# Kernel optimization log

Measured on AMD Instinct MI355X. Metric: run time of the kernel, lower is better.

Reference implementation:

```python
import jax, jax.numpy as jnp
import numpy as np

N_NODES = 50000
N_EDGES = 1600000
N_PAIRS = 4096
IN_N, IN_E = 32, 8
H, OE, ON = 4, 8, 32  # heads, out_edge_feats, out_node_feats
L = 4  # layers


def setup_inputs() -> dict:
    key = jax.random.key(0)
    ks = jax.random.split(key, 20)
    s = 0.1
    return {
        "x": jax.random.normal(ks[0], (N_NODES, IN_N), jnp.float32),
        "e": jax.random.normal(ks[1], (N_EDGES, IN_E), jnp.float32),
        "W_ni": jax.random.normal(ks[2], (L, IN_N, H * OE), jnp.float32) * s,
        "W_nj": jax.random.normal(ks[3], (L, IN_N, H * OE), jnp.float32) * s,
        "W_fij": jax.random.normal(ks[4], (L, IN_E, H * OE), jnp.float32) * s,
        "b_edge": jax.random.normal(ks[5], (L, H * OE), jnp.float32) * s,
        "attn": jax.random.normal(ks[6], (L, H, OE), jnp.float32) * s,
        "W_node": jax.random.normal(ks[7], (L, IN_N, H * ON), jnp.float32) * s,
        "W1": jax.random.normal(ks[8], (2 * L * ON, 128), jnp.float32) * s,
        "b1": jax.random.normal(ks[9], (128,), jnp.float32) * s,
        "W2": jax.random.normal(ks[10], (128, 1), jnp.float32) * s,
        "b2": jax.random.normal(ks[11], (1,), jnp.float32) * s,
        "src": jax.random.randint(ks[12], (N_EDGES,), 0, N_NODES, jnp.int32),
        "dst": jax.random.randint(ks[13], (N_EDGES,), 0, N_NODES, jnp.int32),
        "users": jax.random.randint(ks[14], (N_PAIRS,), 0, N_NODES, jnp.int32),
        "items": jax.random.randint(ks[15], (N_PAIRS,), 0, N_NODES, jnp.int32),
    }


def _egat_layer(h, e, src, dst, W_ni, W_nj, W_fij, b_edge, attn, W_node, n_nodes):
    # per-edge edge features: f_ni[src] + f_nj[dst] + f_fij + bias  -> (E, H*OE)
    f = (h @ W_ni)[src] + (h @ W_nj)[dst] + e @ W_fij + b_edge
    f_out = jax.nn.leaky_relu(f).reshape(-1, H, OE)          # (E, H, OE)
    logits = jnp.einsum("ehd,hd->eh", f_out, attn)           # (E, H)
    # edge softmax over incoming edges of each dst node
    mx = jax.ops.segment_max(logits, dst, num_segments=n_nodes)
    z = jnp.exp(logits - mx[dst])
    denom = jax.ops.segment_sum(z, dst, num_segments=n_nodes)
    a = z / denom[dst]                                        # (E, H)
    hh = (h @ W_node).reshape(n_nodes, H, ON)                 # (N, H, ON)
    msg = hh[src] * a[:, :, None]                             # (E, H, ON)
    return jax.ops.segment_sum(msg, dst, num_segments=n_nodes)  # (N, H, ON)


def reference(x, e, W_ni, W_nj, W_fij, b_edge, attn, W_node, W1, b1, W2, b2,
              src, dst, users, items):
    n_nodes = x.shape[0]
    states = []
    h = x
    for l in range(L):
        agg = _egat_layer(h, e, src, dst, W_ni[l], W_nj[l], W_fij[l],
                          b_edge[l], attn[l], W_node[l], n_nodes)
        h = jax.nn.elu(agg.sum(axis=1))  # sum heads, ELU -> (N, ON)
        states.append(h)
    states = jnp.concatenate(states, axis=1)                  # (N, L*ON)
    z = jnp.concatenate([states[users], states[items]], axis=1)  # (B, 2*L*ON)
    z = jax.nn.relu(z @ W1 + b1)
    out = jax.nn.sigmoid(z @ W2 + b2)
    return out[:, 0]
```

## Files before the change

kernel.cpp:

```cpp
#include <hip/hip_runtime.h>
#include <math.h>


static __device__ inline unsigned short f2bf(float f) {
  unsigned x = __float_as_uint(f);
  unsigned r = x + 0x7fffu + ((x >> 16) & 1u);
  return (unsigned short)(r >> 16);
}
static __device__ inline unsigned pack2bf(float lo, float hi) {
  return (unsigned)f2bf(lo) | ((unsigned)f2bf(hi) << 16);
}
static __device__ inline float bf_lo(unsigned u) {
  return __uint_as_float(u << 16);
}
static __device__ inline float bf_hi(unsigned u) {
  return __uint_as_float(u & 0xffff0000u);
}


__global__ void zero_ints(int* __restrict__ p, int n) {
  int i = blockIdx.x * blockDim.x + threadIdx.x;
  if (i < n) p[i] = 0;
}

__global__ void histogram(const int* __restrict__ dst, int* __restrict__ hist,
                          int n_edges) {
  int e = blockIdx.x * blockDim.x + threadIdx.x;
  if (e < n_edges) atomicAdd(&hist[dst[e]], 1);
}

__global__ void scan_block(const int* __restrict__ hist, int* __restrict__ partial,
                           int* __restrict__ blocksum, int n) {
  __shared__ int buf[1024];
  int tid = threadIdx.x;
  int g = blockIdx.x * 1024 + tid;
  int v = (g < n) ? hist[g] : 0;
  buf[tid] = v;
  __syncthreads();
  for (int off = 1; off < 1024; off <<= 1) {
    int t = (tid >= off) ? buf[tid - off] : 0;
    __syncthreads();
    buf[tid] += t;
    __syncthreads();
  }
  if (g < n) partial[g] = buf[tid] - v;
  if (tid == 1023) blocksum[blockIdx.x] = buf[1023];
}

__global__ void scan_sums(int* __restrict__ blocksum, int nb) {
  if (threadIdx.x == 0 && blockIdx.x == 0) {
    int run = 0;
    for (int i = 0; i < nb; i++) {
      int t = blocksum[i];
      blocksum[i] = run;
      run += t;
    }
    blocksum[nb] = run;
  }
}

__global__ void scan_add(int* __restrict__ partial ,
                         const int* __restrict__ blocksum,
                         int* __restrict__ cursor, int n, int nb) {
  int g = blockIdx.x * blockDim.x + threadIdx.x;
  if (g < n) {
    int val = partial[g] + blocksum[g >> 10];
    partial[g] = val;
    cursor[g] = val;
  }
  if (g == 0) partial[n] = blocksum[nb];
}

#define FILL_NR 8
__global__ void fill_rec(const int* __restrict__ dst, const int* __restrict__ src,
                         int* __restrict__ cursor, int2* __restrict__ rec,
                         int n_edges, int seg) {
  int range = blockIdx.x % FILL_NR;
  int group = blockIdx.x / FILL_NR;
  int ngroups = gridDim.x / FILL_NR;
  int lo = range * seg;
  int hi = lo + seg;
  int stride = ngroups * blockDim.x;
  for (int k = group * blockDim.x + threadIdx.x; k < n_edges; k += stride) {
    int d = dst[k];
    if (d >= lo && d < hi) {
      int p = atomicAdd(&cursor[d], 1);
      rec[p] = make_int2(src[k], k);
    }
  }
}

__global__ void dst_fill(const int* __restrict__ row_off, int* __restrict__ dst_s,
                         int n_nodes) {
  int n = blockIdx.x * blockDim.x + threadIdx.x;
  if (n >= n_nodes) return;
  int b = row_off[n], e = row_off[n + 1];
  for (int k = b; k < e; k++) dst_s[k] = n;
}

__global__ void expand_e(const int2* __restrict__ rec, const float* __restrict__ e,
                         uint4* __restrict__ e_s, int n_edges) {
  int k = blockIdx.x * blockDim.x + threadIdx.x;
  if (k >= n_edges) return;
  int eid = rec[k].y;
  const float4* ep = (const float4*)(e + (size_t)eid * 8);
  float4 a = ep[0], b = ep[1];
  uint4 r;
  r.x = pack2bf(a.x, a.y); r.y = pack2bf(a.z, a.w);
  r.z = pack2bf(b.x, b.y); r.w = pack2bf(b.z, b.w);
  e_s[k] = r;
}


__global__ void node_proj(const float* __restrict__ h,
                          const float* __restrict__ Wni,
                          const float* __restrict__ Wnj,
                          const float* __restrict__ Wnode,
                          const float* __restrict__ bE,
                          unsigned short* __restrict__ fni,
                          unsigned short* __restrict__ cdst,
                          unsigned short* __restrict__ hh, int n_nodes) {
  int wave = (blockIdx.x * blockDim.x + threadIdx.x) >> 6;
  int lane = threadIdx.x & 63;
  int nwaves = (gridDim.x * blockDim.x) >> 6;
  int j = lane & 31;
  const float* Wsel = (lane < 32) ? Wni : Wnj;
  for (int n = wave; n < n_nodes; n += nwaves) {
    const float* hrow = h + (size_t)n * 32;
    float a0 = 0.f, a1 = 0.f, a2 = 0.f;
#pragma unroll
    for (int k = 0; k < 32; k++) {
      float hv = hrow[k];
      a0 += hv * Wsel[k * 32 + j];
      a1 += hv * Wnode[k * 128 + lane];
      a2 += hv * Wnode[k * 128 + lane + 64];
    }
    if (lane < 32) fni[(size_t)n * 32 + j] = f2bf(a0);
    else           cdst[(size_t)n * 32 + j] = f2bf(a0 + bE[j]);
    hh[(size_t)n * 128 + lane] = f2bf(a1);
    hh[(size_t)n * 128 + lane + 64] = f2bf(a2);
  }
}

__global__ void edge_z(const int2* __restrict__ rec,
                       const int* __restrict__ dst_s,
                       const uint4* __restrict__ e_s,
                       const unsigned short* __restrict__ fni,
                       const unsigned short* __restrict__ cdst,
                       const float* __restrict__ Wf,
                       const float* __restrict__ attn,
                       float4* __restrict__ zrec, int n_edges) {
  __shared__ float wfl[256];
  __shared__ float atl[32];
  int tid = threadIdx.x;
  wfl[tid] = Wf[tid];
  if (tid < 32) atl[tid] = attn[tid];
  __syncthreads();
  int k = blockIdx.x * blockDim.x + tid;
  if (k >= n_edges) return;
  int s = rec[k].x, d = dst_s[k];
  uint4 ep = e_s[k];
  float ev[8];
  ev[0] = bf_lo(ep.x); ev[1] = bf_hi(ep.x);
  ev[2] = bf_lo(ep.y); ev[3] = bf_hi(ep.y);
  ev[4] = bf_lo(ep.z); ev[5] = bf_hi(ep.z);
  ev[6] = bf_lo(ep.w); ev[7] = bf_hi(ep.w);
  const uint4* fr = (const uint4*)(fni + (size_t)s * 32);
  const uint4* cr = (const uint4*)(cdst + (size_t)d * 32);
  float f[32];
#pragma unroll
  for (int q = 0; q < 4; q++) {
    uint4 ua = fr[q], ub = cr[q];
    const unsigned* uap = (const unsigned*)&ua;
    const unsigned* ubp = (const unsigned*)&ub;
#pragma unroll
    for (int c = 0; c < 4; c++) {
      int jj = q * 8 + c * 2;
      f[jj]     = bf_lo(uap[c]) + bf_lo(ubp[c]);
      f[jj + 1] = bf_hi(uap[c]) + bf_hi(ubp[c]);
    }
  }
#pragma unroll
  for (int kk = 0; kk < 8; kk++) {
    float ek = ev[kk];
#pragma unroll
    for (int j4 = 0; j4 < 8; j4++) {
      float4 w = ((const float4*)wfl)[kk * 8 + j4];
      f[j4 * 4 + 0] = fmaf(ek, w.x, f[j4 * 4 + 0]);
      f[j4 * 4 + 1] = fmaf(ek, w.y, f[j4 * 4 + 1]);
      f[j4 * 4 + 2] = fmaf(ek, w.z, f[j4 * 4 + 2]);
      f[j4 * 4 + 3] = fmaf(ek, w.w, f[j4 * 4 + 3]);
    }
  }
  float lg[4] = {0.f, 0.f, 0.f, 0.f};
#pragma unroll
  for (int jj = 0; jj < 32; jj++) {
    float t = f[jj];
    t = (t >= 0.f) ? t : 0.01f * t;
    lg[jj >> 3] = fmaf(t, atl[jj], lg[jj >> 3]);
  }
  zrec[k] = make_float4(__expf(lg[0]), __expf(lg[1]),
                        __expf(lg[2]), __expf(lg[3]));
}

__global__ void node_agg(const float4* __restrict__ zrec,
                         const int2* __restrict__ rec,
                         const int* __restrict__ row_off,
                         const unsigned* __restrict__ hh,
                         float* __restrict__ hcur,
                         float* __restrict__ states,
                         int l, int n_nodes) {
  __shared__ float zw[4][64 * 4];
  __shared__ int sw[4][64];
  int wid = threadIdx.x >> 6;
  int lane = threadIdx.x & 63;
  int n = (blockIdx.x * blockDim.x + threadIdx.x) >> 6;
  if (n >= n_nodes) return;
  int base = row_off[n], end = row_off[n + 1];
  int head = lane >> 4;
  float* zwf = zw[wid];
  int* swp = sw[wid];
  float accx = 0.f, accy = 0.f;
  float sz0 = 0.f, sz1 = 0.f, sz2 = 0.f, sz3 = 0.f;

  for (int chunk = base; chunk < end; chunk += 64) {
    int k = chunk + lane;
    float4 zv4 = make_float4(0.f, 0.f, 0.f, 0.f);
    int sv = 0;
    if (k < end) { zv4 = zrec[k]; sv = rec[k].x; }
    ((float4*)zwf)[lane] = zv4;
    swp[lane] = sv;
    sz0 += zv4.x; sz1 += zv4.y; sz2 += zv4.z; sz3 += zv4.w;
    int cnt = min(64, end - chunk);

    int ee = 0;
    for (; ee + 8 <= cnt; ee += 8) {
      unsigned u[8];
      float zl[8];
#pragma unroll
      for (int i = 0; i < 8; i++) {
        int ss = __builtin_amdgcn_readfirstlane(swp[ee + i]);
        zl[i] = zwf[(ee + i) * 4 + head];
        u[i] = hh[(size_t)ss * 64 + lane];
      }
#pragma unroll
      for (int i = 0; i < 8; i++) {
        accx = fmaf(bf_lo(u[i]), zl[i], accx);
        accy = fmaf(bf_hi(u[i]), zl[i], accy);
      }
    }
    for (; ee < cnt; ee++) {
      int ss = __builtin_amdgcn_readfirstlane(swp[ee]);
      float zv = zwf[ee * 4 + head];
      unsigned u = hh[(size_t)ss * 64 + lane];
      accx = fmaf(bf_lo(u), zv, accx);
      accy = fmaf(bf_hi(u), zv, accy);
    }
  }

#pragma unroll
  for (int off = 32; off > 0; off >>= 1) {
    sz0 += __shfl_xor(sz0, off); sz1 += __shfl_xor(sz1, off);
    sz2 += __shfl_xor(sz2, off); sz3 += __shfl_xor(sz3, off);
  }
  float dh = (head == 0) ? sz0 : (head == 1) ? sz1 : (head == 2) ? sz2 : sz3;

  float vx = 0.f, vy = 0.f;
  if (dh > 0.f) { vx = accx / dh; vy = accy / dh; }
  vx += __shfl_xor(vx, 16); vx += __shfl_xor(vx, 32);
  vy += __shfl_xor(vy, 16); vy += __shfl_xor(vy, 32);
  if (lane < 16) {
    float rx = (vx > 0.f) ? vx : expm1f(vx);
    float ry = (vy > 0.f) ? vy : expm1f(vy);
    float2 r = make_float2(rx, ry);
    ((float2*)(hcur + (size_t)n * 32))[lane] = r;
    ((float2*)(states + (size_t)n * 128 + l * 32))[lane] = r;
  }
}

__global__ void mlp_head(const float* __restrict__ states,
                         const int* __restrict__ users, const int* __restrict__ items,
                         const float* __restrict__ W1, const float* __restrict__ b1,
                         const float* __restrict__ W2, const float* __restrict__ b2,
                         float* __restrict__ out, int n_pairs) {
  __shared__ float zin[256];
  __shared__ float red[2];
  int p = blockIdx.x;
  if (p >= n_pairs) return;
  int t = threadIdx.x;
  int u = users[p], it = items[p];
  zin[t] = states[(size_t)u * 128 + t];
  zin[t + 128] = states[(size_t)it * 128 + t];
  __syncthreads();
  float acc = b1[t];
#pragma unroll 8
  for (int i = 0; i < 256; i++) acc += zin[i] * W1[i * 128 + t];
  acc = acc > 0.f ? acc : 0.f;
  float c = acc * W2[t];
#pragma unroll
  for (int off = 32; off > 0; off >>= 1) c += __shfl_down(c, off);
  if ((t & 63) == 0) red[t >> 6] = c;
  __syncthreads();
  if (t == 0) {
    float sum = red[0] + red[1] + b2[0];
    out[p] = 1.f / (1.f + expf(-sum));
  }
}


extern "C" void kernel_launch(void* const* d_in, const int* in_sizes, int n_in,
                              void* d_out, int out_size, void* d_ws, size_t ws_size,
                              hipStream_t stream) {
  const float* x     = (const float*)d_in[0];
  const float* e     = (const float*)d_in[1];
  const float* W_ni  = (const float*)d_in[2];
  const float* W_nj  = (const float*)d_in[3];
  const float* W_fij = (const float*)d_in[4];
  const float* b_e   = (const float*)d_in[5];
  const float* attn  = (const float*)d_in[6];
  const float* W_nd  = (const float*)d_in[7];
  const float* W1    = (const float*)d_in[8];
  const float* b1    = (const float*)d_in[9];
  const float* W2    = (const float*)d_in[10];
  const float* b2    = (const float*)d_in[11];
  const int* src   = (const int*)d_in[12];
  const int* dst   = (const int*)d_in[13];
  const int* users = (const int*)d_in[14];
  const int* items = (const int*)d_in[15];
  float* out = (float*)d_out;

  int n_nodes = in_sizes[0] / 32;
  int n_edges = in_sizes[12];
  int n_pairs = in_sizes[14];

  char* wsb = (char*)d_ws;
  size_t off = 0;
  auto alloc = [&](size_t bytes) {
    char* p = wsb + off;
    off = (off + bytes + 255) & ~(size_t)255;
    return p;
  };
  float*          hcur   = (float*)alloc((size_t)n_nodes * 32 * 4);
  float*          states = (float*)alloc((size_t)n_nodes * 128 * 4);
  unsigned short* fni    = (unsigned short*)alloc((size_t)n_nodes * 32 * 2);
  unsigned short* cdst   = (unsigned short*)alloc((size_t)n_nodes * 32 * 2);
  unsigned short* hh     = (unsigned short*)alloc((size_t)n_nodes * 128 * 2);
  uint4*          e_s    = (uint4*)alloc((size_t)n_edges * 16);
  float4*         zrec   = (float4*)alloc((size_t)n_edges * 16);
  int2*           rec    = (int2*)alloc((size_t)n_edges * 8);
  int*            dst_s  = (int*)alloc((size_t)n_edges * 4);
  int*            row_off  = (int*)alloc(((size_t)n_nodes + 8) * 4);
  int*            blocksum = (int*)alloc(256 * 4);
  int* hist   = (int*)zrec;
  int* cursor = (int*)((char*)zrec + (size_t)(n_nodes + 16) * 4);

  int nb = (n_nodes + 1023) / 1024;
  int seg = (n_nodes + FILL_NR - 1) / FILL_NR;
  zero_ints<<<(n_nodes + 255) / 256, 256, 0, stream>>>(hist, n_nodes);
  histogram<<<(n_edges + 255) / 256, 256, 0, stream>>>(dst, hist, n_edges);
  scan_block<<<nb, 1024, 0, stream>>>(hist, row_off, blocksum, n_nodes);
  scan_sums<<<1, 64, 0, stream>>>(blocksum, nb);
  scan_add<<<(n_nodes + 255) / 256, 256, 0, stream>>>(row_off, blocksum, cursor,
                                                      n_nodes, nb);
  fill_rec<<<2048, 256, 0, stream>>>(dst, src, cursor, rec, n_edges, seg);
  dst_fill<<<(n_nodes + 255) / 256, 256, 0, stream>>>(row_off, dst_s, n_nodes);
  expand_e<<<(n_edges + 255) / 256, 256, 0, stream>>>(rec, e, e_s, n_edges);

  for (int l = 0; l < 4; l++) {
    const float* hin = (l == 0) ? x : hcur;
    node_proj<<<2048, 256, 0, stream>>>(hin, W_ni + l * 1024, W_nj + l * 1024,
                                        W_nd + l * 4096, b_e + l * 32,
                                        fni, cdst, hh, n_nodes);
    edge_z<<<(n_edges + 255) / 256, 256, 0, stream>>>(
        rec, dst_s, e_s, fni, cdst, W_fij + l * 256, attn + l * 32,
        zrec, n_edges);
    node_agg<<<(n_nodes * 64 + 255) / 256, 256, 0, stream>>>(
        zrec, rec, row_off, (const unsigned*)hh, hcur, states, l, n_nodes);
  }
  mlp_head<<<n_pairs, 128, 0, stream>>>(states, users, items, W1, b1, W2, b2,
                                        out, n_pairs);
}
```

Measured before the change: 870.7 us.

## Store edge softmax weights as fp16, use nontemporal streaming accesses, halve fill ranges

Per-edge exp(logit) values are stored as packed fp16 instead of fp32, halving zrec traffic between edge_z and node_agg. Streaming per-edge loads and stores (rec, dst_s, e_s, e, zrec) switch to nontemporal builtins so they do not pollute cache. The fill_rec range count drops from 8 to 4, so each edge array is scanned fewer times. fp16 exp values risk overflow or precision loss when logits are large, and nontemporal hints may hurt if the data would otherwise be reused from L2.

```diff
diff --git a/kernel.cpp b/kernel.cpp
--- a/kernel.cpp
+++ b/kernel.cpp
@@ -1,6 +1,10 @@
 #include <hip/hip_runtime.h>
+#include <hip/hip_fp16.h>
 #include <math.h>
 
+
+typedef unsigned uv2 __attribute__((ext_vector_type(2)));
+typedef unsigned uv4 __attribute__((ext_vector_type(4)));
 
 static __device__ inline unsigned short f2bf(float f) {
   unsigned x = __float_as_uint(f);
@@ -15,6 +19,16 @@
 }
 static __device__ inline float bf_hi(unsigned u) {
   return __uint_as_float(u & 0xffff0000u);
+}
+static __device__ inline unsigned pack2h(float a, float b) {
+  __half2 h2 = __floats2half2_rn(a, b);
+  return *(unsigned*)&h2;
+}
+static __device__ inline float h_lo(unsigned u) {
+  return __half2float(__ushort_as_half((unsigned short)(u & 0xffffu)));
+}
+static __device__ inline float h_hi(unsigned u) {
+  return __half2float(__ushort_as_half((unsigned short)(u >> 16)));
 }
 
 
@@ -71,7 +85,7 @@
   if (g == 0) partial[n] = blocksum[nb];
 }
 
-#define FILL_NR 8
+#define FILL_NR 4
 __global__ void fill_rec(const int* __restrict__ dst, const int* __restrict__ src,
                          int* __restrict__ cursor, int2* __restrict__ rec,
                          int n_edges, int seg) {
@@ -99,16 +113,24 @@
 }
 
 __global__ void expand_e(const int2* __restrict__ rec, const float* __restrict__ e,
-                         uint4* __restrict__ e_s, int n_edges) {
+                         uv4* __restrict__ e_s, int n_edges) {
   int k = blockIdx.x * blockDim.x + threadIdx.x;
   if (k >= n_edges) return;
-  int eid = rec[k].y;
-  const float4* ep = (const float4*)(e + (size_t)eid * 8);
-  float4 a = ep[0], b = ep[1];
-  uint4 r;
-  r.x = pack2bf(a.x, a.y); r.y = pack2bf(a.z, a.w);
-  r.z = pack2bf(b.x, b.y); r.w = pack2bf(b.z, b.w);
-  e_s[k] = r;
+  uv2 rc = __builtin_nontemporal_load((const uv2*)rec + k);
+  int eid = (int)rc.y;
+  const float* ep = e + (size_t)eid * 8;
+  float v0 = __builtin_nontemporal_load(ep + 0);
+  float v1 = __builtin_nontemporal_load(ep + 1);
+  float v2 = __builtin_nontemporal_load(ep + 2);
+  float v3 = __builtin_nontemporal_load(ep + 3);
+  float v4 = __builtin_nontemporal_load(ep + 4);
+  float v5 = __builtin_nontemporal_load(ep + 5);
+  float v6 = __builtin_nontemporal_load(ep + 6);
+  float v7 = __builtin_nontemporal_load(ep + 7);
+  uv4 r;
+  r.x = pack2bf(v0, v1); r.y = pack2bf(v2, v3);
+  r.z = pack2bf(v4, v5); r.w = pack2bf(v6, v7);
+  __builtin_nontemporal_store(r, e_s + k);
 }
 
 
@@ -144,12 +166,12 @@
 
 __global__ void edge_z(const int2* __restrict__ rec,
                        const int* __restrict__ dst_s,
-                       const uint4* __restrict__ e_s,
+                       const uv4* __restrict__ e_s,
                        const unsigned short* __restrict__ fni,
                        const unsigned short* __restrict__ cdst,
                        const float* __restrict__ Wf,
                        const float* __restrict__ attn,
-                       float4* __restrict__ zrec, int n_edges) {
+                       uv2* __restrict__ zrec, int n_edges) {
   __shared__ float wfl[256];
   __shared__ float atl[32];
   int tid = threadIdx.x;
@@ -158,8 +180,10 @@
   __syncthreads();
   int k = blockIdx.x * blockDim.x + tid;
   if (k >= n_edges) return;
-  int s = rec[k].x, d = dst_s[k];
-  uint4 ep = e_s[k];
+  uv2 rc = __builtin_nontemporal_load((const uv2*)rec + k);
+  int s = (int)rc.x;
+  int d = __builtin_nontemporal_load(dst_s + k);
+  uv4 ep = __builtin_nontemporal_load(e_s + k);
   float ev[8];
   ev[0] = bf_lo(ep.x); ev[1] = bf_hi(ep.x);
   ev[2] = bf_lo(ep.y); ev[3] = bf_hi(ep.y);
@@ -199,11 +223,13 @@
     t = (t >= 0.f) ? t : 0.01f * t;
     lg[jj >> 3] = fmaf(t, atl[jj], lg[jj >> 3]);
   }
-  zrec[k] = make_float4(__expf(lg[0]), __expf(lg[1]),
-                        __expf(lg[2]), __expf(lg[3]));
-}
-
-__global__ void node_agg(const float4* __restrict__ zrec,
+  uv2 zout;
+  zout.x = pack2h(__expf(lg[0]), __expf(lg[1]));
+  zout.y = pack2h(__expf(lg[2]), __expf(lg[3]));
+  __builtin_nontemporal_store(zout, zrec + k);
+}
+
+__global__ void node_agg(const uv2* __restrict__ zrec,
                          const int2* __restrict__ rec,
                          const int* __restrict__ row_off,
                          const unsigned* __restrict__ hh,
@@ -227,7 +253,12 @@
     int k = chunk + lane;
     float4 zv4 = make_float4(0.f, 0.f, 0.f, 0.f);
     int sv = 0;
-    if (k < end) { zv4 = zrec[k]; sv = rec[k].x; }
+    if (k < end) {
+      uv2 zz = __builtin_nontemporal_load(zrec + k);
+      zv4 = make_float4(h_lo(zz.x), h_hi(zz.x), h_lo(zz.y), h_hi(zz.y));
+      uv2 rc = __builtin_nontemporal_load((const uv2*)rec + k);
+      sv = (int)rc.x;
+    }
     ((float4*)zwf)[lane] = zv4;
     swp[lane] = sv;
     sz0 += zv4.x; sz1 += zv4.y; sz2 += zv4.z; sz3 += zv4.w;
@@ -345,8 +376,8 @@
   unsigned short* fni    = (unsigned short*)alloc((size_t)n_nodes * 32 * 2);
   unsigned short* cdst   = (unsigned short*)alloc((size_t)n_nodes * 32 * 2);
   unsigned short* hh     = (unsigned short*)alloc((size_t)n_nodes * 128 * 2);
-  uint4*          e_s    = (uint4*)alloc((size_t)n_edges * 16);
-  float4*         zrec   = (float4*)alloc((size_t)n_edges * 16);
+  uv4*            e_s    = (uv4*)alloc((size_t)n_edges * 16);
+  uv2*            zrec   = (uv2*)alloc((size_t)n_edges * 8);
   int2*           rec    = (int2*)alloc((size_t)n_edges * 8);
   int*            dst_s  = (int*)alloc((size_t)n_edges * 4);
   int*            row_off  = (int*)alloc(((size_t)n_nodes + 8) * 4);
```

Measured after the change: 886.5 us. No clear change (+1.8%).
